# Kernel optimization log

Measured on AMD Instinct MI355X. Metric: run time of the kernel, lower is better.

Reference implementation:

```python
import jax, jax.numpy as jnp
import numpy as np

DIM = 1024
HEADS = 16
HEAD_DIM = DIM // HEADS  # 64
EPS = 1e-5


def layer_norm(x, w, b):
    # LayerNorm over last dim (head_dim), matching nn.LayerNorm defaults
    mu = jnp.mean(x, axis=-1, keepdims=True)
    var = jnp.mean(jnp.square(x - mu), axis=-1, keepdims=True)
    return (x - mu) * jax.lax.rsqrt(var + EPS) * w + b


def apply_rotary_emb(x, freqs):
    # x: [B, S, H, D]; freqs: [S, D/2] angles. Interleaved (complex) rotary:
    # pairs (x[2i], x[2i+1]) rotated by angle freqs[:, i].
    x1 = x[..., 0::2]
    x2 = x[..., 1::2]
    cos = jnp.cos(freqs)[None, :, None, :]
    sin = jnp.sin(freqs)[None, :, None, :]
    r1 = x1 * cos - x2 * sin
    r2 = x1 * sin + x2 * cos
    return jnp.stack([r1, r2], axis=-1).reshape(x.shape)


def setup_inputs() -> dict:
    key = jax.random.key(0)
    ks = jax.random.split(key, 8)
    B, S = 2, 2048
    x = jax.random.normal(ks[0], (B, S, DIM), dtype=jnp.float32)
    freqs = jax.random.uniform(ks[1], (S, HEAD_DIM // 2), dtype=jnp.float32)
    sc = 1.0 / np.sqrt(DIM)
    w_qkv = jax.random.normal(ks[2], (DIM, 4 * DIM), dtype=jnp.float32) * sc
    w_out = jax.random.normal(ks[3], (DIM, DIM), dtype=jnp.float32) * sc
    qn_w = jnp.ones((HEAD_DIM,), jnp.float32)
    qn_b = jnp.zeros((HEAD_DIM,), jnp.float32)
    kn_w = jnp.ones((HEAD_DIM,), jnp.float32)
    kn_b = jnp.zeros((HEAD_DIM,), jnp.float32)
    return {"x": x, "freqs": freqs, "w_qkv": w_qkv, "w_out": w_out,
            "qn_w": qn_w, "qn_b": qn_b, "kn_w": kn_w, "kn_b": kn_b}


def reference(x, freqs, w_qkv, w_out, qn_w, qn_b, kn_w, kn_b):
    B, S, _ = x.shape
    qkv = x @ w_qkv  # [B, S, 4*DIM]
    q, k, v, gate = jnp.split(qkv, 4, axis=-1)
    q = q.reshape(B, S, HEADS, HEAD_DIM)
    k = k.reshape(B, S, HEADS, HEAD_DIM)
    v = v.reshape(B, S, HEADS, HEAD_DIM)
    q = layer_norm(q, qn_w, qn_b)
    k = layer_norm(k, kn_w, kn_b)
    q = apply_rotary_emb(q, freqs)
    k = apply_rotary_emb(k, freqs)
    # flash_attn_func: non-causal softmax attention, scale 1/sqrt(head_dim)
    scale = 1.0 / np.sqrt(HEAD_DIM)
    scores = jnp.einsum('bqhd,bkhd->bhqk', q, k) * scale
    probs = jax.nn.softmax(scores, axis=-1)
    o = jnp.einsum('bhqk,bkhd->bqhd', probs, v)
    o = o.reshape(B, S, DIM)
    o = o * jax.nn.sigmoid(gate)
    return o @ w_out
```

## Files before the change

kernel.cpp:

```cpp
#include <hip/hip_runtime.h>


typedef _Float16 f16;
typedef _Float16 f16x8 __attribute__((ext_vector_type(8)));
typedef _Float16 f16x4 __attribute__((ext_vector_type(4)));
typedef float    f32x4 __attribute__((ext_vector_type(4)));

#define MFMA16(a, b, c) __builtin_amdgcn_mfma_f32_16x16x32_f16((a), (b), (c), 0, 0, 0)

__device__ __forceinline__ void gload16(const void* g, void* l) {
  __builtin_amdgcn_global_load_lds(
      (const __attribute__((address_space(1))) void*)g,
      (__attribute__((address_space(3))) void*)l, 16, 0, 0);
}

__device__ __forceinline__ float exp2_fast(float x) {
#if __has_builtin(__builtin_amdgcn_exp2f)
  return __builtin_amdgcn_exp2f(x);
#else
  float r;
  asm("v_exp_f32 %0, %1" : "=v"(r) : "v"(x));
  return r;
#endif
}
__device__ __forceinline__ unsigned pkrtz(float a, float b) {
  typedef __fp16 hf16x2 __attribute__((ext_vector_type(2)));
  union { hf16x2 h; unsigned u; } c;
  c.h = __builtin_amdgcn_cvt_pkrtz(a, b);
  return c.u;
}

__global__ void rope_table_kernel(const float* __restrict__ freqs, float* __restrict__ tbl) {
  int i = blockIdx.x * 256 + threadIdx.x;
  if (i >= 2048 * 32) return;
  int s = i >> 5, j = i & 31;
  float f = freqs[i];
  tbl[s * 64 + j]      = cosf(f);
  tbl[s * 64 + 32 + j] = sinf(f);
}

__global__ void cast_f16_kernel(const float* __restrict__ in, f16* __restrict__ out, int n8) {
  int i = blockIdx.x * 256 + threadIdx.x;
  if (i >= n8) return;
  float4 a = ((const float4*)in)[2 * i];
  float4 b = ((const float4*)in)[2 * i + 1];
  f16x8 o;
  o[0] = (f16)a.x; o[1] = (f16)a.y; o[2] = (f16)a.z; o[3] = (f16)a.w;
  o[4] = (f16)b.x; o[5] = (f16)b.y; o[6] = (f16)b.z; o[7] = (f16)b.w;
  ((f16x8*)out)[i] = o;
}

__global__ void transpose_cast_kernel(const float* __restrict__ in, f16* __restrict__ out,
                                      int R, int C) {
  __shared__ float t[64][65];
  int c0 = blockIdx.x * 64, r0 = blockIdx.y * 64;
  int tx = threadIdx.x & 15, ty = threadIdx.x >> 4;
#pragma unroll
  for (int i = 0; i < 4; ++i) {
    float4 v = *(const float4*)&in[(size_t)(r0 + ty + 16 * i) * C + c0 + tx * 4];
    t[ty + 16 * i][tx * 4 + 0] = v.x;
    t[ty + 16 * i][tx * 4 + 1] = v.y;
    t[ty + 16 * i][tx * 4 + 2] = v.z;
    t[ty + 16 * i][tx * 4 + 3] = v.w;
  }
  __syncthreads();
#pragma unroll
  for (int i = 0; i < 4; ++i) {
    int n = c0 + ty + 16 * i;
    int k = r0 + tx * 4;
    f16x4 o;
    o[0] = (f16)t[tx * 4 + 0][ty + 16 * i];
    o[1] = (f16)t[tx * 4 + 1][ty + 16 * i];
    o[2] = (f16)t[tx * 4 + 2][ty + 16 * i];
    o[3] = (f16)t[tx * 4 + 3][ty + 16 * i];
    *(f16x4*)&out[(size_t)n * R + k] = o;
  }
}

__global__ void fill_debug_kernel(float* out, int n) {
  int i = blockIdx.x * 256 + threadIdx.x;
  if (i < n) out[i] = 12345.0f;
}

template <int EPI>
__global__ __launch_bounds__(256, 2) void gemm_f16(
    const f16* __restrict__ A, const f16* __restrict__ B,
    float* __restrict__ Cout, int M, int N, int K,
    float* __restrict__ q_f32, float* __restrict__ k_f32,
    float* __restrict__ gate_f32, f16* __restrict__ v_t) {
  __shared__ f16 sA[128 * 64], sB[128 * 64];
  const int tid = threadIdx.x, lane = tid & 63;
  const int wave = tid >> 6, wm = wave >> 1, wn = wave & 1;
  const int lg = lane >> 4, lr = lane & 15;
  const int n0 = blockIdx.x * 128, m0 = blockIdx.y * 128;

  f32x4 acc[4][4];
#pragma unroll
  for (int m = 0; m < 4; ++m)
#pragma unroll
    for (int n = 0; n < 4; ++n) acc[m][n] = (f32x4){0.f, 0.f, 0.f, 0.f};

  for (int k0 = 0; k0 < K; k0 += 64) {
#pragma unroll
    for (int r = 0; r < 4; ++r) {
      int off = (tid + r * 256) * 16;
      int row = off >> 7;
      int col = ((off & 127) ^ ((row & 7) << 4)) >> 1;
      gload16(A + (size_t)(m0 + row) * K + k0 + col, (char*)sA + off);
      gload16(B + (size_t)(n0 + row) * K + k0 + col, (char*)sB + off);
    }
    __syncthreads();
#pragma unroll
    for (int ks = 0; ks < 2; ++ks) {
      f16x8 bfr[4];
#pragma unroll
      for (int n = 0; n < 4; ++n) {
        int row = wn * 64 + n * 16 + lr;
        int boff = (row << 7) + (ks << 6) + (lg << 4);
        boff ^= (row & 7) << 4;
        bfr[n] = *(const f16x8*)((const char*)sB + boff);
      }
#pragma unroll
      for (int m = 0; m < 4; ++m) {
        int row = wm * 64 + m * 16 + lr;
        int aoff = (row << 7) + (ks << 6) + (lg << 4);
        aoff ^= (row & 7) << 4;
        f16x8 afr = *(const f16x8*)((const char*)sA + aoff);
#pragma unroll
        for (int n = 0; n < 4; ++n) acc[m][n] = MFMA16(afr, bfr[n], acc[m][n]);
      }
    }
    __syncthreads();
  }

  if (EPI == 0) {
#pragma unroll
    for (int m = 0; m < 4; ++m) {
      int row = m0 + wm * 64 + m * 16 + 4 * lg;
#pragma unroll
      for (int n = 0; n < 4; ++n) {
        int col = n0 + wn * 64 + n * 16 + lr;
#pragma unroll
        for (int r = 0; r < 4; ++r) Cout[(size_t)(row + r) * N + col] = acc[m][n][r];
      }
    }
  } else {
    int region = n0 >> 10;
#pragma unroll
    for (int m = 0; m < 4; ++m) {
      int row = m0 + wm * 64 + m * 16 + 4 * lg;
#pragma unroll
      for (int n = 0; n < 4; ++n) {
        int col = n0 + wn * 64 + n * 16 + lr;
        if (region == 0) {
#pragma unroll
          for (int r = 0; r < 4; ++r) q_f32[(size_t)(row + r) * 1024 + col] = acc[m][n][r];
        } else if (region == 1) {
#pragma unroll
          for (int r = 0; r < 4; ++r) k_f32[(size_t)(row + r) * 1024 + col - 1024] = acc[m][n][r];
        } else if (region == 3) {
#pragma unroll
          for (int r = 0; r < 4; ++r) gate_f32[(size_t)(row + r) * 1024 + col - 3072] = acc[m][n][r];
        } else {
          int c = col - 2048, hh = c >> 6, d = c & 63;
          int b = row >> 11, s = row & 2047;
          f16x4 pv;
          pv[0] = (f16)acc[m][n][0];
          pv[1] = (f16)acc[m][n][1];
          pv[2] = (f16)acc[m][n][2];
          pv[3] = (f16)acc[m][n][3];
          *(f16x4*)&v_t[(size_t)((b * 16 + hh) * 64 + d) * 2048 + s] = pv;
        }
      }
    }
  }
}

__global__ void norm_rope_kernel(const float* __restrict__ qf, const float* __restrict__ kf,
                                 const float* __restrict__ tbl,
                                 const float* __restrict__ qn_w, const float* __restrict__ qn_b,
                                 const float* __restrict__ kn_w, const float* __restrict__ kn_b,
                                 f16* __restrict__ q_h, f16* __restrict__ k_h) {
  int row = blockIdx.x;
  int s = row & 2047;
  int hh = threadIdx.x >> 4, sub = threadIdx.x & 15;
  int base = row * 1024 + hh * 64 + sub * 4;
  float c0 = tbl[s * 64 + sub * 2 + 0], c1 = tbl[s * 64 + sub * 2 + 1];
  float s0 = tbl[s * 64 + 32 + sub * 2 + 0], s1 = tbl[s * 64 + 32 + sub * 2 + 1];
#pragma unroll
  for (int which = 0; which < 2; ++which) {
    const float* src = which ? kf : qf;
    const float* wp = which ? kn_w : qn_w;
    const float* bp = which ? kn_b : qn_b;
    f16* dst = which ? k_h : q_h;
    float4 x = *(const float4*)&src[base];
    float sum = x.x + x.y + x.z + x.w;
    sum += __shfl_xor(sum, 1); sum += __shfl_xor(sum, 2);
    sum += __shfl_xor(sum, 4); sum += __shfl_xor(sum, 8);
    float mu = sum * (1.0f / 64.0f);
    float d0 = x.x - mu, d1 = x.y - mu, d2 = x.z - mu, d3 = x.w - mu;
    float sq = d0 * d0 + d1 * d1 + d2 * d2 + d3 * d3;
    sq += __shfl_xor(sq, 1); sq += __shfl_xor(sq, 2);
    sq += __shfl_xor(sq, 4); sq += __shfl_xor(sq, 8);
    float rstd = rsqrtf(sq * (1.0f / 64.0f) + 1e-5f);
    float4 w = *(const float4*)&wp[sub * 4];
    float4 bb = *(const float4*)&bp[sub * 4];
    float n0 = d0 * rstd * w.x + bb.x;
    float n1 = d1 * rstd * w.y + bb.y;
    float n2 = d2 * rstd * w.z + bb.z;
    float n3 = d3 * rstd * w.w + bb.w;
    float r0 = n0 * c0 - n1 * s0, r1 = n0 * s0 + n1 * c0;
    float r2 = n2 * c1 - n3 * s1, r3 = n2 * s1 + n3 * c1;
    f16x4 ov;
    ov[0] = (f16)r0; ov[1] = (f16)r1; ov[2] = (f16)r2; ov[3] = (f16)r3;
    *(f16x4*)&dst[base] = ov;
  }
}

__global__ __launch_bounds__(256, 2) void attn_kernel(const f16* __restrict__ q_h,
                                                      const f16* __restrict__ k_h,
                                                      const f16* __restrict__ v_t,
                                                      const float* __restrict__ gate_f32,
                                                      f16* __restrict__ a16) {
  __shared__ __align__(16) char smem[65536];
  const int tid = threadIdx.x, lane = tid & 63, wave = tid >> 6;
  const int lg = lane >> 4, lr = lane & 15;
  const int bh = blockIdx.x >> 4, qt = blockIdx.x & 15;
  const int b = bh >> 4, h = bh & 15;
  const int qrow0 = b * 2048 + qt * 128 + wave * 32;

  auto stage = [&](int kv0, int p) {
    char* kb = smem + p * 16384;
    char* vb = smem + 32768 + p * 16384;
#pragma unroll
    for (int r = 0; r < 4; ++r) {
      int off = (tid + r * 256) * 16;
      {
        int row = off >> 7;
        int col = ((off & 127) ^ ((row & 7) << 4)) >> 1;
        gload16(&k_h[(size_t)(b * 2048 + kv0 + row) * 1024 + h * 64 + col], kb + off);
      }
      {
        int d = off >> 8;
        int col = ((off & 255) ^ ((d & 15) << 4)) >> 1;
        gload16(&v_t[(size_t)(bh * 64 + d) * 2048 + kv0 + col], vb + off);
      }
    }
  };

  f16x8 qf[2][2];
#pragma unroll
  for (int n = 0; n < 2; ++n)
#pragma unroll
    for (int ks = 0; ks < 2; ++ks)
      qf[n][ks] = *(const f16x8*)&q_h[(size_t)(qrow0 + n * 16 + lr) * 1024 + h * 64 + ks * 32 + lg * 8];

  f16x8 ones;
#pragma unroll
  for (int j = 0; j < 8; ++j) ones[j] = (f16)1.0f;

  f32x4 accO[4][2];
#pragma unroll
  for (int m = 0; m < 4; ++m) {
    accO[m][0] = (f32x4){0.f, 0.f, 0.f, 0.f};
    accO[m][1] = (f32x4){0.f, 0.f, 0.f, 0.f};
  }
  f32x4 accL[2] = {(f32x4){0.f, 0.f, 0.f, 0.f}, (f32x4){0.f, 0.f, 0.f, 0.f}};
  float mrun[2] = {-1e30f, -1e30f};
  const float SCL2 = 0.125f * 1.44269504f;

  stage(0, 0);

  int cur = 0;
  for (int t = 0; t < 16; ++t, cur ^= 1) {
    __syncthreads();
    if (t < 15) stage((t + 1) * 128, cur ^ 1);

    const char* kb = smem + cur * 16384;
    const char* vb = smem + 32768 + cur * 16384;

    f32x4 st[8][2];
#pragma unroll
    for (int m = 0; m < 8; ++m) {
      st[m][0] = (f32x4){0.f, 0.f, 0.f, 0.f};
      st[m][1] = (f32x4){0.f, 0.f, 0.f, 0.f};
    }
    __builtin_amdgcn_s_setprio(1);
#pragma unroll
    for (int m = 0; m < 8; ++m)
#pragma unroll
      for (int ks = 0; ks < 2; ++ks) {
        int row = m * 16 + lr;
        int koff = (row << 7) + (ks << 6) + (lg << 4);
        koff ^= (row & 7) << 4;
        f16x8 a = *(const f16x8*)(kb + koff);
        st[m][0] = MFMA16(a, qf[0][ks], st[m][0]);
        st[m][1] = MFMA16(a, qf[1][ks], st[m][1]);
      }
    __builtin_amdgcn_s_setprio(0);

    uint2 pdw[2][8];
#pragma unroll
    for (int n = 0; n < 2; ++n) {
      float vm = st[0][n][0];
#pragma unroll
      for (int m = 0; m < 8; ++m)
#pragma unroll
        for (int r = 0; r < 4; ++r)
          if (m | r) vm = fmaxf(vm, st[m][n][r]);
      vm = fmaxf(vm, __shfl_xor(vm, 16));
      vm = fmaxf(vm, __shfl_xor(vm, 32));
      if (__any(vm > mrun[n])) {
        float mnew = fmaxf(mrun[n], vm);
        float fac = exp2_fast((mrun[n] - mnew) * SCL2);
        mrun[n] = mnew;
        accL[n] *= fac;
#pragma unroll
        for (int m = 0; m < 4; ++m) accO[m][n] *= fac;
      }
      float mc = mrun[n] * SCL2;
#pragma unroll
      for (int m = 0; m < 8; ++m) {
        float p0 = exp2_fast(st[m][n][0] * SCL2 - mc);
        float p1 = exp2_fast(st[m][n][1] * SCL2 - mc);
        float p2 = exp2_fast(st[m][n][2] * SCL2 - mc);
        float p3 = exp2_fast(st[m][n][3] * SCL2 - mc);
        pdw[n][m].x = pkrtz(p0, p1);
        pdw[n][m].y = pkrtz(p2, p3);
      }
    }

    char* pb_lds = (char*)kb + wave * 4096;
#pragma unroll
    for (int half = 0; half < 2; ++half) {
      asm volatile("s_waitcnt lgkmcnt(0)" ::: "memory");
#pragma unroll
      for (int n = 0; n < 2; ++n) {
        int q = n * 16 + lr;
#pragma unroll
        for (int mm = 0; mm < 4; ++mm) {
          int poff = (q << 7) + (mm << 5) + (lg << 3);
          poff ^= (q & 7) << 4;
          *(uint2*)(pb_lds + poff) = pdw[n][half * 4 + mm];
        }
      }
      asm volatile("s_waitcnt lgkmcnt(0)" ::: "memory");
      __builtin_amdgcn_sched_barrier(0);

      f16x8 pb[2][2];
#pragma unroll
      for (int n = 0; n < 2; ++n) {
        int q = n * 16 + lr;
#pragma unroll
        for (int ksl = 0; ksl < 2; ++ksl) {
          int poff = (q << 7) + (ksl << 6) + (lg << 4);
          poff ^= (q & 7) << 4;
          pb[n][ksl] = *(const f16x8*)(pb_lds + poff);
        }
      }
      __builtin_amdgcn_s_setprio(1);
#pragma unroll
      for (int m = 0; m < 4; ++m)
#pragma unroll
        for (int ksl = 0; ksl < 2; ++ksl) {
          int ks = half * 2 + ksl;
          int d = m * 16 + lr;
          int voff = (d << 8) + (ks << 6) + (lg << 4);
          voff ^= (d & 15) << 4;
          f16x8 av = *(const f16x8*)(vb + voff);
          accO[m][0] = MFMA16(av, pb[0][ksl], accO[m][0]);
          accO[m][1] = MFMA16(av, pb[1][ksl], accO[m][1]);
        }
#pragma unroll
      for (int ksl = 0; ksl < 2; ++ksl) {
        accL[0] = MFMA16(ones, pb[0][ksl], accL[0]);
        accL[1] = MFMA16(ones, pb[1][ksl], accL[1]);
      }
      __builtin_amdgcn_s_setprio(0);
    }
  }

#pragma unroll
  for (int n = 0; n < 2; ++n) {
    float rl = 1.0f / accL[n][0];
    int orow = qrow0 + n * 16 + lr;
#pragma unroll
    for (int m = 0; m < 4; ++m) {
      size_t idx = (size_t)orow * 1024 + h * 64 + m * 16 + lg * 4;
      float4 gv = *(const float4*)&gate_f32[idx];
      f16x4 ov;
      ov[0] = (f16)(accO[m][n][0] * rl / (1.f + __expf(-gv.x)));
      ov[1] = (f16)(accO[m][n][1] * rl / (1.f + __expf(-gv.y)));
      ov[2] = (f16)(accO[m][n][2] * rl / (1.f + __expf(-gv.z)));
      ov[3] = (f16)(accO[m][n][3] * rl / (1.f + __expf(-gv.w)));
      *(f16x4*)&a16[idx] = ov;
    }
  }
}

extern "C" void kernel_launch(void* const* d_in, const int* in_sizes, int n_in,
                              void* d_out, int out_size, void* d_ws, size_t ws_size,
                              hipStream_t stream) {
  const float* x      = (const float*)d_in[0];
  const float* freqs  = (const float*)d_in[1];
  const float* w_qkv  = (const float*)d_in[2];
  const float* w_out  = (const float*)d_in[3];
  const float* qn_w   = (const float*)d_in[4];
  const float* qn_b   = (const float*)d_in[5];
  const float* kn_w   = (const float*)d_in[6];
  const float* kn_b   = (const float*)d_in[7];
  float* out = (float*)d_out;
  char* ws = (char*)d_ws;
  const size_t MB = 1024 * 1024;
  float* q_f32    = (float*)(ws + 0);
  float* k_f32    = (float*)(ws + 16 * MB);
  float* gate_f32 = (float*)(ws + 32 * MB);
  f16*   v_t      = (f16*)(ws + 48 * MB);
  f16*   x16      = (f16*)(ws + 56 * MB);
  f16*   wq16     = (f16*)(ws + 64 * MB);
  f16*   wo16     = (f16*)(ws + 72 * MB);
  f16*   q_h      = (f16*)(ws + 74 * MB);
  f16*   k_h      = (f16*)(ws + 82 * MB);
  float* tbl      = (float*)(ws + 90 * MB);
  f16*   a16      = x16;

  if (ws_size < (size_t)91 * MB) {
    fill_debug_kernel<<<(out_size + 255) / 256, 256, 0, stream>>>(out, out_size);
    return;
  }

  rope_table_kernel<<<256, 256, 0, stream>>>(freqs, tbl);
  cast_f16_kernel<<<2048, 256, 0, stream>>>(x, x16, 524288);
  transpose_cast_kernel<<<dim3(64, 16), 256, 0, stream>>>(w_qkv, wq16, 1024, 4096);
  transpose_cast_kernel<<<dim3(16, 16), 256, 0, stream>>>(w_out, wo16, 1024, 1024);

  gemm_f16<1><<<dim3(32, 32), 256, 0, stream>>>(x16, wq16, nullptr, 4096, 4096, 1024,
                                                q_f32, k_f32, gate_f32, v_t);
  norm_rope_kernel<<<4096, 256, 0, stream>>>(q_f32, k_f32, tbl, qn_w, qn_b, kn_w, kn_b, q_h, k_h);
  attn_kernel<<<512, 256, 0, stream>>>(q_h, k_h, v_t, gate_f32, a16);
  gemm_f16<0><<<dim3(8, 32), 256, 0, stream>>>(a16, wo16, out, 4096, 1024, 1024,
                                               nullptr, nullptr, nullptr, nullptr);
}
```

Measured before the change: 161.3 us.

## Permute K rows at load so P stays in registers for PV MFMA

K tile rows are loaded into LDS in a permuted order, so the S accumulator layout from QK^T lines up with the B-operand layout the PV MFMA expects. The probabilities can then be packed straight from registers into f16x8 operands, with no LDS write and read-back. This drops two lgkmcnt waits, a sched barrier and the LDS traffic for P on every KV tile. It relies on the row permutation matching the MFMA lane layout exactly; any mismatch would give wrong results.

```diff
diff --git a/kernel.cpp b/kernel.cpp
--- a/kernel.cpp
+++ b/kernel.cpp
@@ -238,7 +238,8 @@
       {
         int row = off >> 7;
         int col = ((off & 127) ^ ((row & 7) << 4)) >> 1;
-        gload16(&k_h[(size_t)(b * 2048 + kv0 + row) * 1024 + h * 64 + col], kb + off);
+        int g = ((row >> 5) << 5) + (((row >> 2) & 3) << 3) + (((row >> 4) & 1) << 2) + (row & 3);
+        gload16(&k_h[(size_t)(b * 2048 + kv0 + g) * 1024 + h * 64 + col], kb + off);
       }
       {
         int d = off >> 8;
@@ -330,54 +331,34 @@
       }
     }
 
-    char* pb_lds = (char*)kb + wave * 4096;
-#pragma unroll
-    for (int half = 0; half < 2; ++half) {
-      asm volatile("s_waitcnt lgkmcnt(0)" ::: "memory");
-#pragma unroll
-      for (int n = 0; n < 2; ++n) {
-        int q = n * 16 + lr;
-#pragma unroll
-        for (int mm = 0; mm < 4; ++mm) {
-          int poff = (q << 7) + (mm << 5) + (lg << 3);
-          poff ^= (q & 7) << 4;
-          *(uint2*)(pb_lds + poff) = pdw[n][half * 4 + mm];
-        }
-      }
-      asm volatile("s_waitcnt lgkmcnt(0)" ::: "memory");
-      __builtin_amdgcn_sched_barrier(0);
-
-      f16x8 pb[2][2];
-#pragma unroll
-      for (int n = 0; n < 2; ++n) {
-        int q = n * 16 + lr;
-#pragma unroll
-        for (int ksl = 0; ksl < 2; ++ksl) {
-          int poff = (q << 7) + (ksl << 6) + (lg << 4);
-          poff ^= (q & 7) << 4;
-          pb[n][ksl] = *(const f16x8*)(pb_lds + poff);
-        }
-      }
-      __builtin_amdgcn_s_setprio(1);
-#pragma unroll
-      for (int m = 0; m < 4; ++m)
-#pragma unroll
-        for (int ksl = 0; ksl < 2; ++ksl) {
-          int ks = half * 2 + ksl;
-          int d = m * 16 + lr;
-          int voff = (d << 8) + (ks << 6) + (lg << 4);
-          voff ^= (d & 15) << 4;
-          f16x8 av = *(const f16x8*)(vb + voff);
-          accO[m][0] = MFMA16(av, pb[0][ksl], accO[m][0]);
-          accO[m][1] = MFMA16(av, pb[1][ksl], accO[m][1]);
-        }
-#pragma unroll
-      for (int ksl = 0; ksl < 2; ++ksl) {
-        accL[0] = MFMA16(ones, pb[0][ksl], accL[0]);
-        accL[1] = MFMA16(ones, pb[1][ksl], accL[1]);
-      }
-      __builtin_amdgcn_s_setprio(0);
-    }
+    f16x8 pb[2][4];
+#pragma unroll
+    for (int n = 0; n < 2; ++n)
+#pragma unroll
+      for (int ks = 0; ks < 4; ++ks) {
+        union { uint4 u; f16x8 h; } c;
+        c.u = make_uint4(pdw[n][2 * ks].x, pdw[n][2 * ks].y,
+                         pdw[n][2 * ks + 1].x, pdw[n][2 * ks + 1].y);
+        pb[n][ks] = c.h;
+      }
+    __builtin_amdgcn_s_setprio(1);
+#pragma unroll
+    for (int m = 0; m < 4; ++m)
+#pragma unroll
+      for (int ks = 0; ks < 4; ++ks) {
+        int d = m * 16 + lr;
+        int voff = (d << 8) + (ks << 6) + (lg << 4);
+        voff ^= (d & 15) << 4;
+        f16x8 av = *(const f16x8*)(vb + voff);
+        accO[m][0] = MFMA16(av, pb[0][ks], accO[m][0]);
+        accO[m][1] = MFMA16(av, pb[1][ks], accO[m][1]);
+      }
+#pragma unroll
+    for (int ks = 0; ks < 4; ++ks) {
+      accL[0] = MFMA16(ones, pb[0][ks], accL[0]);
+      accL[1] = MFMA16(ones, pb[1][ks], accL[1]);
+    }
+    __builtin_amdgcn_s_setprio(0);
   }
 
 #pragma unroll
```

New measurement: 155.5 us. 1.04x faster.
